# Kernel tuning notes

Hardware: AMD Instinct MI355X
Metric: run time of the kernel (lower is better)

Reference implementation:

```python
import jax, jax.numpy as jnp
import numpy as np

B, N, C_CLASS, C_CHARGE, S_MAX = 128, 256, 5, 3, 300


def setup_inputs() -> dict:
    key = jax.random.key(0)
    ks = jax.random.split(key, 12)
    return {
        "particle_class": jax.random.randint(ks[0], (B, N), 0, C_CLASS),
        "particle_charge": jax.random.randint(ks[1], (B, N), 0, C_CHARGE),
        "n_particles": jax.random.randint(ks[2], (B,), 0, S_MAX),
        "pflow_class_logits": jax.random.normal(ks[3], (B, N, C_CLASS), jnp.float32),
        "pflow_charge_logits": jax.random.normal(ks[4], (B, N, C_CHARGE), jnp.float32),
        "particle_pos": jax.random.normal(ks[5], (B, N, 3), jnp.float32),
        "pflow_pos": jax.random.normal(ks[6], (B, N, 3), jnp.float32),
        "particle_mom": jax.random.normal(ks[7], (B, N, 3), jnp.float32),
        "pflow_mom": jax.random.normal(ks[8], (B, N, 3), jnp.float32),
        "particle_energy": jax.random.normal(ks[9], (B, N), jnp.float32),
        "pflow_energy": jax.random.normal(ks[10], (B, N), jnp.float32),
        "predicted_setsizes": jax.random.normal(ks[11], (B, N, S_MAX), jnp.float32),
    }


def _pairwise_nll(logits, labels):
    # logits: [B, Nq, C] (pflow/dst side), labels: [B, Np] int (particle/src side)
    # returns CE(dst_logits_j, src_label_i) for every pair -> [B, Np, Nq]
    logp = jax.nn.log_softmax(logits, axis=-1)            # [B, Nq, C]
    idx = labels[:, :, None, None]                        # [B, Np, 1, 1]
    return -jnp.take_along_axis(logp[:, None, :, :], idx, axis=3)[..., 0]


def reference(particle_class, particle_charge, n_particles,
              pflow_class_logits, pflow_charge_logits,
              particle_pos, pflow_pos, particle_mom, pflow_mom,
              particle_energy, pflow_energy, predicted_setsizes):
    # per-edge (full bipartite per event) pair losses -> [B, Np, Nq]
    class_l = _pairwise_nll(pflow_class_logits, particle_class)
    charge_l = _pairwise_nll(pflow_charge_logits, particle_charge)
    pos_l = jnp.linalg.norm(particle_pos[:, :, None, :] - pflow_pos[:, None, :, :], axis=-1)
    mom_l = jnp.linalg.norm(particle_mom[:, :, None, :] - pflow_mom[:, None, :, :], axis=-1)
    en_l = (particle_energy[:, :, None] - pflow_energy[:, None, :]) ** 2
    pair_loss = class_l + charge_l + pos_l + mom_l + en_l  # [B, Np, Nq]

    # segment-min over mailbox: per-pflow min over incoming particle edges,
    # per-particle min over incoming pflow edges
    min_per_pflow = pair_loss.min(axis=1)      # [B, Nq]
    min_per_particle = pair_loss.min(axis=2)   # [B, Np]

    particle_loss = min_per_particle.sum(axis=1).mean()
    pflow_loss = min_per_pflow.sum(axis=1).mean()

    # setsize: mean over pflow nodes per event, CE against true multiplicity
    setsize_logp = jax.nn.log_softmax(predicted_setsizes.mean(axis=1), axis=-1)  # [B, S]
    setsize_loss = -jnp.take_along_axis(setsize_logp, n_particles[:, None], axis=1)[:, 0].mean()

    loss = particle_loss + pflow_loss + setsize_loss
    return loss
```

## Files before the change

### kernel.cpp

```cpp
#include <hip/hip_runtime.h>
#include <math.h>

#define BQ 128
#define NQ 256
#define SMAX 300
#define CCLS 5
#define CCHG 3
#define TSTR 268
#define RSTR 12
#define INFV 3.0e38f

#define NPAIR 256
#define NMAIN (NPAIR + BQ)

__device__ __forceinline__ float fast_sqrtf(float x) {
    return __builtin_amdgcn_sqrtf(x);
}

#define P_TAB   0
#define P_COLS  4020
#define P_ROWS  6068
#define P_RED   7604
#define P_PART  9652
#define SMEM_FLOATS 9656


__global__ __launch_bounds__(512, 2) void main_kernel(
    const int* __restrict__ p_class, const int* __restrict__ p_charge,
    const int* __restrict__ n_particles,
    const float* __restrict__ cls_logits, const float* __restrict__ chg_logits,
    const float* __restrict__ p_pos, const float* __restrict__ pf_pos,
    const float* __restrict__ p_mom, const float* __restrict__ pf_mom,
    const float* __restrict__ p_en, const float* __restrict__ pf_en,
    const float* __restrict__ setsizes, float* __restrict__ ws,
    float* __restrict__ out)
{
    __shared__ float smem[SMEM_FLOATS];
    const int t = threadIdx.x;
    const int blk = blockIdx.x;

    if (blk < NPAIR) {
        const int b  = blk >> 1;
        const int rh = blk & 1;
        const int base = b * NQ;
        float* s_tab  = smem + P_TAB;
        float* s_cols = smem + P_COLS;
        float* s_rows = smem + P_ROWS;
        float* s_red  = smem + P_RED;
        float* s_part = smem + P_PART;

        if (t < NQ) {
            const int gj = base + t;
            const float* cl = cls_logits + (size_t)gj * CCLS;
            float l0=cl[0], l1=cl[1], l2=cl[2], l3=cl[3], l4=cl[4];
            float mx = fmaxf(fmaxf(fmaxf(l0,l1),fmaxf(l2,l3)),l4);
            float lse = mx + __logf(__expf(l0-mx)+__expf(l1-mx)+__expf(l2-mx)+
                                    __expf(l3-mx)+__expf(l4-mx));
            const float* gl = chg_logits + (size_t)gj * CCHG;
            float g0=gl[0], g1=gl[1], g2=gl[2];
            float gmx = fmaxf(fmaxf(g0,g1),g2);
            float glse = gmx + __logf(__expf(g0-gmx)+__expf(g1-gmx)+__expf(g2-gmx));
            float nc[CCLS] = {lse-l0, lse-l1, lse-l2, lse-l3, lse-l4};
            float ng[CCHG] = {glse-g0, glse-g1, glse-g2};
            #pragma unroll
            for (int c = 0; c < CCLS; ++c)
                #pragma unroll
                for (int g = 0; g < CCHG; ++g)
                    s_tab[(c*CCHG+g)*TSTR + t] = nc[c] + ng[g];

            float* cr = &s_cols[t*8];
            cr[0]=pf_pos[gj*3+0]; cr[1]=pf_pos[gj*3+1]; cr[2]=pf_pos[gj*3+2];
            cr[3]=pf_mom[gj*3+0]; cr[4]=pf_mom[gj*3+1]; cr[5]=pf_mom[gj*3+2];
            cr[6]=pf_en[gj];      cr[7]=0.0f;
        } else if (t < NQ + 128) {
            const int rr = t - NQ;
            const int gr = base + rh*128 + rr;
            float* rw = &s_rows[rr*RSTR];
            rw[0]=p_pos[gr*3+0]; rw[1]=p_pos[gr*3+1]; rw[2]=p_pos[gr*3+2];
            rw[3]=p_mom[gr*3+0]; rw[4]=p_mom[gr*3+1]; rw[5]=p_mom[gr*3+2];
            rw[6]=p_en[gr];
            rw[7]=__int_as_float(p_class[gr]*CCHG + p_charge[gr]);
        }
        __syncthreads();

        const int tx = t & 31;
        const int ty = t >> 5;
        const int c0 = ty * 16;

        float4 ra[4], rb[4];
        int ccr[4];
        #pragma unroll
        for (int r = 0; r < 4; ++r) {
            const int row = tx + 32*r;
            ra[r] = *(const float4*)&s_rows[row*RSTR];
            rb[r] = *(const float4*)&s_rows[row*RSTR + 4];
            ccr[r] = __float_as_int(rb[r].w) * TSTR;
        }
        float cmin[16];
        #pragma unroll
        for (int c = 0; c < 16; ++c) cmin[c] = INFV;
        float rmin[4] = {INFV, INFV, INFV, INFV};

        #pragma unroll 4
        for (int c = 0; c < 16; ++c) {
            const int j = c0 + c;
            const float4 cd0 = *(const float4*)&s_cols[j*8];
            const float4 cd1 = *(const float4*)&s_cols[j*8+4];
            float cm = cmin[c];
            #pragma unroll
            for (int r = 0; r < 4; ++r) {
                float dx=ra[r].x-cd0.x, dy=ra[r].y-cd0.y, dz=ra[r].z-cd0.z;
                float ex=ra[r].w-cd0.w, ey=rb[r].x-cd1.x, ez=rb[r].y-cd1.y;
                float de=rb[r].z-cd1.z;
                float v = s_tab[ccr[r] + j]
                        + fast_sqrtf(dx*dx + dy*dy + dz*dz)
                        + fast_sqrtf(ex*ex + ey*ey + ez*ez)
                        + de*de;
                rmin[r] = fminf(rmin[r], v);
                cm = fminf(cm, v);
            }
            cmin[c] = cm;
        }

        #pragma unroll 4
        for (int c = 0; c < 16; ++c) {
            float v = cmin[c];
            #pragma unroll
            for (int off = 16; off > 0; off >>= 1)
                v = fminf(v, __shfl_down(v, off, 32));
            if (tx == 0) ws[blk*NQ + c0 + c] = v;
        }
        #pragma unroll
        for (int r = 0; r < 4; ++r)
            s_red[ty*128 + tx + 32*r] = rmin[r];
        __syncthreads();

        if (t < 128) {
            float m = s_red[t];
            #pragma unroll
            for (int k = 1; k < 16; ++k) m = fminf(m, s_red[k*128 + t]);
            #pragma unroll
            for (int off = 32; off > 0; off >>= 1) m += __shfl_down(m, off, 64);
            if ((t & 63) == 0) s_part[t >> 6] = m;
        }
        __syncthreads();
        if (t == 0)
            atomicAdd(out, (s_part[0] + s_part[1]) * (1.0f / BQ));

    } else {
        const int b = blk - NPAIR;
        float* s_ss = smem;
        float* s_m  = smem + 608;
        float* s_p5 = smem + 912;
        float* s_one= smem + 920;

        const int slice = t >> 8;
        const int col = t & 255;
        const float* bp = setsizes + (size_t)b * NQ * SMAX + (size_t)(slice*128) * SMAX;
        {
            const float* p = bp + col;
            float acc = 0.f;
            #pragma unroll 16
            for (int i = 0; i < 128; ++i) acc += p[(size_t)i * SMAX];
            s_ss[slice*304 + col] = acc;
        }
        if (col < SMAX - NQ) {
            const float* p = bp + (NQ + col);
            float acc = 0.f;
            #pragma unroll 16
            for (int i = 0; i < 128; ++i) acc += p[(size_t)i * SMAX];
            s_ss[slice*304 + NQ + col] = acc;
        }
        __syncthreads();
        float m = -INFV;
        if (t < SMAX) { m = (s_ss[t] + s_ss[304 + t]) * (1.0f / NQ); s_m[t] = m; }
        const int wave = t >> 6, lane = t & 63;
        float wm = m;
        #pragma unroll
        for (int off = 32; off > 0; off >>= 1) wm = fmaxf(wm, __shfl_down(wm, off));
        if (lane == 0 && wave < 5) s_p5[wave] = wm;
        __syncthreads();
        if (t == 0)
            s_one[0] = fmaxf(fmaxf(fmaxf(s_p5[0], s_p5[1]), fmaxf(s_p5[2], s_p5[3])), s_p5[4]);
        __syncthreads();
        const float mx = s_one[0];
        float e = (t < SMAX) ? __expf(m - mx) : 0.f;
        #pragma unroll
        for (int off = 32; off > 0; off >>= 1) e += __shfl_down(e, off);
        if (lane == 0 && wave < 5) s_p5[wave] = e;
        __syncthreads();
        if (t == 0) {
            float s = s_p5[0] + s_p5[1] + s_p5[2] + s_p5[3] + s_p5[4];
            int nb = n_particles[b];
            float loss = -(s_m[nb] - mx - __logf(s));
            atomicAdd(out, loss * (1.0f / BQ));
        }
    }
}

__global__ __launch_bounds__(256) void finish_kernel(
    const float* __restrict__ ws, float* __restrict__ out)
{
    const int b = blockIdx.x;
    const int t = threadIdx.x;
    __shared__ float s_p[4];
    float v = fminf(ws[(b*2)*NQ + t], ws[(b*2+1)*NQ + t]);
    #pragma unroll
    for (int off = 32; off > 0; off >>= 1) v += __shfl_down(v, off, 64);
    if ((t & 63) == 0) s_p[t >> 6] = v;
    __syncthreads();
    if (t == 0)
        atomicAdd(out, (s_p[0] + s_p[1] + s_p[2] + s_p[3]) * (1.0f / BQ));
}

extern "C" void kernel_launch(void* const* d_in, const int* in_sizes, int n_in,
                              void* d_out, int out_size, void* d_ws, size_t ws_size,
                              hipStream_t stream) {
    (void)in_sizes; (void)n_in; (void)ws_size;
    const int*   p_class     = (const int*)d_in[0];
    const int*   p_charge    = (const int*)d_in[1];
    const int*   n_particles = (const int*)d_in[2];
    const float* cls_logits  = (const float*)d_in[3];
    const float* chg_logits  = (const float*)d_in[4];
    const float* p_pos       = (const float*)d_in[5];
    const float* pf_pos      = (const float*)d_in[6];
    const float* p_mom       = (const float*)d_in[7];
    const float* pf_mom      = (const float*)d_in[8];
    const float* p_en        = (const float*)d_in[9];
    const float* pf_en       = (const float*)d_in[10];
    const float* setsizes    = (const float*)d_in[11];
    float* out = (float*)d_out;
    float* ws  = (float*)d_ws;

    (void)hipMemsetAsync(out, 0, sizeof(float) * (size_t)out_size, stream);

    main_kernel<<<NMAIN, 512, 0, stream>>>(
        p_class, p_charge, n_particles, cls_logits, chg_logits,
        p_pos, pf_pos, p_mom, pf_mom, p_en, pf_en, setsizes, ws, out);

    finish_kernel<<<BQ, 256, 0, stream>>>(ws, out);
}
```

Measured before the change: 112.2 us.

## Split setsize reduction into quarter-event blocks interleaved with pair blocks

The setsize column-sum work is now split into four 64-row chunks per event, for 512 small blocks instead of 128 large ones. These blocks are interleaved one-to-two with the pairwise-loss blocks by block index modulo 3, so the memory-bound streaming runs alongside the compute-bound pair work. Partial sums go to workspace, and the log-softmax and cross-entropy move into the finish kernel, which now runs 512 threads per event. This costs extra workspace traffic and more work in the finish kernel, in exchange for better load balance and overlap across CUs.

```diff
diff --git a/kernel.cpp b/kernel.cpp
--- a/kernel.cpp
+++ b/kernel.cpp
@@ -4,14 +4,14 @@
 #define BQ 128
 #define NQ 256
 #define SMAX 300
+#define SPAD 304
 #define CCLS 5
 #define CCHG 3
 #define TSTR 268
 #define RSTR 12
 #define INFV 3.0e38f
 
-#define NPAIR 256
-#define NMAIN (NPAIR + BQ)
+#define NMAIN 768
 
 __device__ __forceinline__ float fast_sqrtf(float x) {
     return __builtin_amdgcn_sqrtf(x);
@@ -24,10 +24,10 @@
 #define P_PART  9652
 #define SMEM_FLOATS 9656
 
+#define WS_SS 65536
 
 __global__ __launch_bounds__(512, 2) void main_kernel(
     const int* __restrict__ p_class, const int* __restrict__ p_charge,
-    const int* __restrict__ n_particles,
     const float* __restrict__ cls_logits, const float* __restrict__ chg_logits,
     const float* __restrict__ p_pos, const float* __restrict__ pf_pos,
     const float* __restrict__ p_mom, const float* __restrict__ pf_mom,
@@ -38,10 +38,12 @@
     __shared__ float smem[SMEM_FLOATS];
     const int t = threadIdx.x;
     const int blk = blockIdx.x;
-
-    if (blk < NPAIR) {
-        const int b  = blk >> 1;
-        const int rh = blk & 1;
+    const int mod3 = blk % 3;
+
+    if (mod3 == 0) {
+        const int pblk = blk / 3;
+        const int b  = pblk >> 1;
+        const int rh = pblk & 1;
         const int base = b * NQ;
         float* s_tab  = smem + P_TAB;
         float* s_cols = smem + P_COLS;
@@ -128,7 +130,7 @@
             #pragma unroll
             for (int off = 16; off > 0; off >>= 1)
                 v = fminf(v, __shfl_down(v, off, 32));
-            if (tx == 0) ws[blk*NQ + c0 + c] = v;
+            if (tx == 0) ws[pblk*NQ + c0 + c] = v;
         }
         #pragma unroll
         for (int r = 0; r < 4; ++r)
@@ -148,69 +150,68 @@
             atomicAdd(out, (s_part[0] + s_part[1]) * (1.0f / BQ));
 
     } else {
-        const int b = blk - NPAIR;
-        float* s_ss = smem;
-        float* s_m  = smem + 608;
-        float* s_p5 = smem + 912;
-        float* s_one= smem + 920;
-
-        const int slice = t >> 8;
-        const int col = t & 255;
-        const float* bp = setsizes + (size_t)b * NQ * SMAX + (size_t)(slice*128) * SMAX;
-        {
-            const float* p = bp + col;
+        const int sblk = (blk / 3) * 2 + (mod3 - 1);
+        const int b  = sblk >> 2;
+        const int ch = sblk & 3;
+        if (t < SMAX) {
+            const float* p = setsizes + ((size_t)b * NQ + (size_t)ch * 64) * SMAX + t;
             float acc = 0.f;
-            #pragma unroll 16
-            for (int i = 0; i < 128; ++i) acc += p[(size_t)i * SMAX];
-            s_ss[slice*304 + col] = acc;
-        }
-        if (col < SMAX - NQ) {
-            const float* p = bp + (NQ + col);
-            float acc = 0.f;
-            #pragma unroll 16
-            for (int i = 0; i < 128; ++i) acc += p[(size_t)i * SMAX];
-            s_ss[slice*304 + NQ + col] = acc;
-        }
-        __syncthreads();
-        float m = -INFV;
-        if (t < SMAX) { m = (s_ss[t] + s_ss[304 + t]) * (1.0f / NQ); s_m[t] = m; }
-        const int wave = t >> 6, lane = t & 63;
-        float wm = m;
-        #pragma unroll
-        for (int off = 32; off > 0; off >>= 1) wm = fmaxf(wm, __shfl_down(wm, off));
-        if (lane == 0 && wave < 5) s_p5[wave] = wm;
-        __syncthreads();
-        if (t == 0)
-            s_one[0] = fmaxf(fmaxf(fmaxf(s_p5[0], s_p5[1]), fmaxf(s_p5[2], s_p5[3])), s_p5[4]);
-        __syncthreads();
-        const float mx = s_one[0];
-        float e = (t < SMAX) ? __expf(m - mx) : 0.f;
-        #pragma unroll
-        for (int off = 32; off > 0; off >>= 1) e += __shfl_down(e, off);
-        if (lane == 0 && wave < 5) s_p5[wave] = e;
-        __syncthreads();
-        if (t == 0) {
-            float s = s_p5[0] + s_p5[1] + s_p5[2] + s_p5[3] + s_p5[4];
-            int nb = n_particles[b];
-            float loss = -(s_m[nb] - mx - __logf(s));
-            atomicAdd(out, loss * (1.0f / BQ));
+            #pragma unroll 8
+            for (int i = 0; i < 64; ++i) acc += p[(size_t)i * SMAX];
+            ws[WS_SS + sblk * SPAD + t] = acc;
         }
     }
 }
 
-__global__ __launch_bounds__(256) void finish_kernel(
-    const float* __restrict__ ws, float* __restrict__ out)
+__global__ __launch_bounds__(512) void finish_kernel(
+    const float* __restrict__ ws, const int* __restrict__ n_particles,
+    float* __restrict__ out)
 {
     const int b = blockIdx.x;
     const int t = threadIdx.x;
-    __shared__ float s_p[4];
-    float v = fminf(ws[(b*2)*NQ + t], ws[(b*2+1)*NQ + t]);
+    __shared__ float s_m[SPAD];
+    __shared__ float s_p[8];
+    __shared__ float s_one[1];
+    const int wave = t >> 6, lane = t & 63;
+
+    float v = 0.f;
+    if (t < NQ)
+        v = fminf(ws[(b*2)*NQ + t], ws[(b*2+1)*NQ + t]);
     #pragma unroll
     for (int off = 32; off > 0; off >>= 1) v += __shfl_down(v, off, 64);
-    if ((t & 63) == 0) s_p[t >> 6] = v;
+    if (lane == 0 && wave < 4) s_p[wave] = v;
+    __syncthreads();
+    float colsum = 0.f;
+    if (t == 0) colsum = s_p[0] + s_p[1] + s_p[2] + s_p[3];
+    __syncthreads();
+
+    float m = -INFV;
+    if (t < SMAX) {
+        const float* p = ws + WS_SS + (size_t)(b*4) * SPAD + t;
+        m = (p[0] + p[SPAD] + p[2*SPAD] + p[3*SPAD]) * (1.0f / NQ);
+        s_m[t] = m;
+    }
+    float wm = m;
+    #pragma unroll
+    for (int off = 32; off > 0; off >>= 1) wm = fmaxf(wm, __shfl_down(wm, off, 64));
+    if (lane == 0 && wave < 5) s_p[wave] = wm;
     __syncthreads();
     if (t == 0)
-        atomicAdd(out, (s_p[0] + s_p[1] + s_p[2] + s_p[3]) * (1.0f / BQ));
+        s_one[0] = fmaxf(fmaxf(fmaxf(s_p[0], s_p[1]), fmaxf(s_p[2], s_p[3])), s_p[4]);
+    __syncthreads();
+    const float mx = s_one[0];
+    float e = (t < SMAX) ? __expf(m - mx) : 0.f;
+    #pragma unroll
+    for (int off = 32; off > 0; off >>= 1) e += __shfl_down(e, off, 64);
+    __syncthreads();
+    if (lane == 0 && wave < 5) s_p[wave] = e;
+    __syncthreads();
+    if (t == 0) {
+        float s = s_p[0] + s_p[1] + s_p[2] + s_p[3] + s_p[4];
+        int nb = n_particles[b];
+        float loss = -(s_m[nb] - mx - __logf(s));
+        atomicAdd(out, (colsum + loss) * (1.0f / BQ));
+    }
 }
 
 extern "C" void kernel_launch(void* const* d_in, const int* in_sizes, int n_in,
@@ -235,8 +236,8 @@
     (void)hipMemsetAsync(out, 0, sizeof(float) * (size_t)out_size, stream);
 
     main_kernel<<<NMAIN, 512, 0, stream>>>(
-        p_class, p_charge, n_particles, cls_logits, chg_logits,
+        p_class, p_charge, cls_logits, chg_logits,
         p_pos, pf_pos, p_mom, pf_mom, p_en, pf_en, setsizes, ws, out);
 
-    finish_kernel<<<BQ, 256, 0, stream>>>(ws, out);
-}
+    finish_kernel<<<BQ, 512, 0, stream>>>(ws, n_particles, out);
+}
```

Measured after the change: 119.1 us. 6.1% more time.
